# Kernel tuning notes

Measured on AMD Instinct MI355X. Metric: run time of the kernel, lower is better.

Reference implementation:

```python
import jax, jax.numpy as jnp
import numpy as np

D = 512    # d_model == EMBED_DIM
H = 8      # nhead
FF = 2048  # dim_feedforward
T, B, S, M = 64, 32, 64, 256
EPS = 1e-5


def setup_inputs() -> dict:
    key = jax.random.key(0)
    ks = iter(jax.random.split(key, 40))
    rn = lambda k, shp, s=0.02: s * jax.random.normal(k, shp, jnp.float32)
    inp = {
        'tgt': jax.random.normal(next(ks), (T, B, D), jnp.float32),
        'memory': jax.random.normal(next(ks), (M, B, D), jnp.float32),
        'semantics': jax.random.normal(next(ks), (B, S, D), jnp.float32),
    }
    for pfx in ('pt', 'sa', 'ca'):  # pre_target, self_attn, cross multihead_attn
        inp[pfx + '_wqkv'] = rn(next(ks), (3 * D, D))
        inp[pfx + '_bqkv'] = jnp.zeros((3 * D,), jnp.float32)
        inp[pfx + '_wo'] = rn(next(ks), (D, D))
        inp[pfx + '_bo'] = jnp.zeros((D,), jnp.float32)
    # relevant_mlp_pre_target: fc0 (2D->D), relu, fc1 (D->D), relu, fc2 (D->1)
    inp['mlp_w0'] = rn(next(ks), (D, 2 * D), float(np.sqrt(2.0 / (2 * D))))
    inp['mlp_b0'] = jnp.zeros((D,), jnp.float32)
    inp['mlp_w1'] = rn(next(ks), (D, D), float(np.sqrt(2.0 / D)))
    inp['mlp_b1'] = jnp.zeros((D,), jnp.float32)
    inp['mlp_w2'] = rn(next(ks), (1, D), float(np.sqrt(2.0 / D)))
    inp['mlp_b2'] = jnp.zeros((1,), jnp.float32)
    inp['ffn_w1'] = rn(next(ks), (FF, D))
    inp['ffn_b1'] = jnp.zeros((FF,), jnp.float32)
    inp['ffn_w2'] = rn(next(ks), (D, FF))
    inp['ffn_b2'] = jnp.zeros((D,), jnp.float32)
    for i in (1, 2, 3):
        inp[f'ln{i}_g'] = jnp.ones((D,), jnp.float32)
        inp[f'ln{i}_b'] = jnp.zeros((D,), jnp.float32)
    return inp


def layernorm(x, g, b):
    mu = jnp.mean(x, -1, keepdims=True)
    var = jnp.var(x, -1, keepdims=True)
    return (x - mu) * jax.lax.rsqrt(var + EPS) * g + b


def mha(q, k, v, wqkv, bqkv, wo, bo):
    # q,k,v: (L, B, D) seq-first, like torch nn.MultiheadAttention
    hd = D // H
    wq, wk, wv = jnp.split(wqkv, 3, axis=0)
    bq, bk, bv = jnp.split(bqkv, 3)
    qh = (q @ wq.T + bq).reshape(q.shape[0], q.shape[1], H, hd)
    kh = (k @ wk.T + bk).reshape(k.shape[0], k.shape[1], H, hd)
    vh = (v @ wv.T + bv).reshape(v.shape[0], v.shape[1], H, hd)
    scale = 1.0 / float(np.sqrt(hd))
    att = jax.nn.softmax(jnp.einsum('qbhd,kbhd->bhqk', qh * scale, kh), axis=-1)
    out = jnp.einsum('bhqk,kbhd->qbhd', att, vh).reshape(q.shape[0], q.shape[1], D)
    return out @ wo.T + bo


def get_relevant_semantic(feats, sem, w0, b0, w1, b1, w2, b2):
    # feats: (B,T,D), sem: (B,S,D). Linear-on-concat == sum of two linears, so we
    # never materialize the (B,T,S,2D) cat tensor; hidden (B,T,S,D) is unavoidable math.
    w0c, w0s = w0[:, :D], w0[:, D:]
    h = (feats @ w0c.T)[:, :, None, :] + (sem @ w0s.T)[:, None, :, :] + b0  # (B,T,S,D)
    h = jax.nn.relu(h)
    h = jax.nn.relu(h @ w1.T + b1)
    scores = h @ w2.T + b2                      # (B,T,S,1)
    a = jax.nn.softmax(scores, axis=2)          # softmax over sem axis
    return jnp.sum(sem[:, None, :, :] * a, axis=2)  # (B,T,D)


def reference(tgt, memory, semantics,
              pt_wqkv, pt_bqkv, pt_wo, pt_bo,
              sa_wqkv, sa_bqkv, sa_wo, sa_bo,
              ca_wqkv, ca_bqkv, ca_wo, ca_bo,
              mlp_w0, mlp_b0, mlp_w1, mlp_b1, mlp_w2, mlp_b2,
              ffn_w1, ffn_b1, ffn_w2, ffn_b2,
              ln1_g, ln1_b, ln2_g, ln2_b, ln3_g, ln3_b):
    # MULTIHEAD_PRE_TARGET branch (eval mode: dropout = identity)
    rel = get_relevant_semantic(jnp.transpose(tgt, (1, 0, 2)), semantics,
                                mlp_w0, mlp_b0, mlp_w1, mlp_b1, mlp_w2, mlp_b2)
    sem_k = jnp.transpose(rel, (1, 0, 2))  # (T,B,D) seq-first key/value
    x = tgt + mha(tgt, sem_k, sem_k, pt_wqkv, pt_bqkv, pt_wo, pt_bo)
    # self attention
    x = layernorm(x + mha(x, x, x, sa_wqkv, sa_bqkv, sa_wo, sa_bo), ln1_g, ln1_b)
    # cross attention over encoder memory
    x = layernorm(x + mha(x, memory, memory, ca_wqkv, ca_bqkv, ca_wo, ca_bo), ln2_g, ln2_b)
    # feed-forward
    ff = jax.nn.relu(x @ ffn_w1.T + ffn_b1) @ ffn_w2.T + ffn_b2
    return layernorm(x + ff, ln3_g, ln3_b)
```

## Files before the change

kernel.cpp:

```cpp
#include <hip/hip_runtime.h>
#include <hip/hip_bf16.h>

#define WS_B 32

typedef __attribute__((ext_vector_type(8))) __bf16 bf16x8;
typedef __attribute__((ext_vector_type(4))) float f32x4;
typedef unsigned short ushort_t;

#define MB(x) ((size_t)(x) << 20)
#define LSTR 40

__device__ __forceinline__ unsigned packpair(float lo, float hi) {
    return ((__float_as_uint(lo) + 0x8000u) >> 16) |
           ((__float_as_uint(hi) + 0x8000u) & 0xffff0000u);
}
__device__ __forceinline__ ushort_t f2bf(float x) {
    return (ushort_t)((__float_as_uint(x) + 0x8000u) >> 16);
}
__device__ __forceinline__ float bf2f(ushort_t u) {
    return __uint_as_float(((unsigned)u) << 16);
}
__device__ __forceinline__ unsigned fuse_word(unsigned f, unsigned s) {
    float lo = __uint_as_float(f << 16) + __uint_as_float(s << 16);
    float hi = __uint_as_float(f & 0xffff0000u) + __uint_as_float(s & 0xffff0000u);
    lo = fmaxf(lo, 0.f);
    hi = fmaxf(hi, 0.f);
    return packpair(lo, hi);
}

struct CvtArgs {
    const float* src[13];
    ushort_t* dst[13];
    int n4[13];
};
__global__ __launch_bounds__(256) void megacvt_kernel(CvtArgs a) {
    const int t = blockIdx.y;
    const int n = a.n4[t];
    const float4* S = (const float4*)a.src[t];
    uint2* D = (uint2*)a.dst[t];
    for (int i = blockIdx.x * 256 + threadIdx.x; i < n; i += gridDim.x * 256) {
        float4 v = S[i];
        uint2 o;
        o.x = packpair(v.x, v.y);
        o.y = packpair(v.z, v.w);
        D[i] = o;
    }
}

struct GemmDesc {
    const ushort_t* A;
    const ushort_t* W;
    const float* bias;
    const float* resid;
    float* C;
    ushort_t* Cb;
    int lda, ldw, ldc, K, relu, nbx, blkStart;
};
struct GemmBatch {
    GemmDesc d[4];
    int nd;
};

__global__ __launch_bounds__(256, 3) void mfma_gemm2(GemmBatch bt) {
    __shared__ ushort_t As[128 * LSTR];
    __shared__ ushort_t Bs[128 * LSTR];
    int di = 0;
#pragma unroll
    for (int i = 1; i < 4; ++i)
        if (i < bt.nd && (int)blockIdx.x >= bt.d[i].blkStart) di = i;
    const GemmDesc g = bt.d[di];
    const int local = blockIdx.x - g.blkStart;
    const int mb = local / g.nbx;
    const int nb = local - mb * g.nbx;

    const int tid = threadIdx.x;
    const int w = tid >> 6, lane = tid & 63;
    const int wm = w & 1, wn = w >> 1;
    const int l15 = lane & 15, quad = lane >> 4;

    const int arow = tid >> 1;
    const int a16 = (tid & 1) * 16;
    const ushort_t* Ap = g.A + (long)(mb * 128 + arow) * g.lda + a16;
    const ushort_t* Bp = g.W + (long)(nb * 128 + arow) * g.ldw + a16;
    ushort_t* Asw = &As[arow * LSTR + a16];
    ushort_t* Bsw = &Bs[arow * LSTR + a16];

    f32x4 acc[4][4];
#pragma unroll
    for (int i = 0; i < 4; ++i)
#pragma unroll
        for (int j = 0; j < 4; ++j) acc[i][j] = (f32x4)0.f;

    uint4 a0 = *(const uint4*)Ap;
    uint4 a1 = *(const uint4*)(Ap + 8);
    uint4 b0 = *(const uint4*)Bp;
    uint4 b1 = *(const uint4*)(Bp + 8);

    for (int k0 = 0; k0 < g.K; k0 += 32) {
        __syncthreads();
        *(uint4*)Asw = a0; *(uint4*)(Asw + 8) = a1;
        *(uint4*)Bsw = b0; *(uint4*)(Bsw + 8) = b1;
        if (k0 + 32 < g.K) {
            a0 = *(const uint4*)(Ap + k0 + 32);
            a1 = *(const uint4*)(Ap + k0 + 40);
            b0 = *(const uint4*)(Bp + k0 + 32);
            b1 = *(const uint4*)(Bp + k0 + 40);
        }
        __syncthreads();
        bf16x8 af[4], bf[4];
#pragma unroll
        for (int mt = 0; mt < 4; ++mt)
            af[mt] = *(const bf16x8*)&As[(wm * 64 + mt * 16 + l15) * LSTR + quad * 8];
#pragma unroll
        for (int nt = 0; nt < 4; ++nt)
            bf[nt] = *(const bf16x8*)&Bs[(wn * 64 + nt * 16 + l15) * LSTR + quad * 8];
#pragma unroll
        for (int mt = 0; mt < 4; ++mt)
#pragma unroll
            for (int nt = 0; nt < 4; ++nt)
                acc[mt][nt] = __builtin_amdgcn_mfma_f32_16x16x32_bf16(
                    af[mt], bf[nt], acc[mt][nt], 0, 0, 0);
    }

#pragma unroll
    for (int nt = 0; nt < 4; ++nt) {
        const int col = nb * 128 + wn * 64 + nt * 16 + l15;
        const float bv = g.bias ? g.bias[col] : 0.f;
#pragma unroll
        for (int mt = 0; mt < 4; ++mt) {
            const int row0 = mb * 128 + wm * 64 + mt * 16 + quad * 4;
#pragma unroll
            for (int rg = 0; rg < 4; ++rg) {
                float v = acc[mt][nt][rg] + bv;
                if (g.relu) v = fmaxf(v, 0.f);
                const long off = (long)(row0 + rg) * g.ldc + col;
                if (g.resid) v += g.resid[off];
                if (g.C) g.C[off] = v;
                if (g.Cb) g.Cb[off] = f2bf(v);
            }
        }
    }
}

__global__ __launch_bounds__(512, 2) void h2score_kernel(
    const ushort_t* __restrict__ Fb,
    const ushort_t* __restrict__ Sb,
    const ushort_t* __restrict__ w1b,
    const float* __restrict__ b1,
    const float* __restrict__ w2,
    float* __restrict__ scores4)
{
    __shared__ ushort_t As[128 * LSTR];
    __shared__ ushort_t Bs[256 * LSTR];
    __shared__ float scred[128 * 4];
    const int tid = threadIdx.x;
    const int mb = blockIdx.x, nb = blockIdx.y;
    const int w = tid >> 6, lane = tid & 63;
    const int wm = w & 1, wn = w >> 1;
    const int l15 = lane & 15, quad = lane >> 4;

    const int arow = tid >> 2, akc = tid & 3;
    const int m_g = mb * 128 + arow;
    const int r = m_g >> 6, s = m_g & 63, bidx = r & 31;
    const ushort_t* Fp = Fb + (long)r * 512 + akc * 8;
    const ushort_t* Sp = Sb + (long)(bidx * 64 + s) * 512 + akc * 8;
    const ushort_t* Bp0 = w1b + (long)(nb * 256 + arow) * 512 + akc * 8;
    const ushort_t* Bp1 = Bp0 + (long)128 * 512;
    ushort_t* Asw  = &As[arow * LSTR + akc * 8];
    ushort_t* Bsw0 = &Bs[arow * LSTR + akc * 8];
    ushort_t* Bsw1 = Bsw0 + 128 * LSTR;

    f32x4 acc[4][4];
#pragma unroll
    for (int i = 0; i < 4; ++i)
#pragma unroll
        for (int j = 0; j < 4; ++j) acc[i][j] = (f32x4)0.f;

    uint4 fa = *(const uint4*)Fp;
    uint4 sa = *(const uint4*)Sp;
    uint4 bb0 = *(const uint4*)Bp0;
    uint4 bb1 = *(const uint4*)Bp1;

    for (int k0 = 0; k0 < 512; k0 += 32) {
        __syncthreads();
        uint4 o;
        o.x = fuse_word(fa.x, sa.x);
        o.y = fuse_word(fa.y, sa.y);
        o.z = fuse_word(fa.z, sa.z);
        o.w = fuse_word(fa.w, sa.w);
        *(uint4*)Asw = o;
        *(uint4*)Bsw0 = bb0;
        *(uint4*)Bsw1 = bb1;
        if (k0 + 32 < 512) {
            fa  = *(const uint4*)(Fp + k0 + 32);
            sa  = *(const uint4*)(Sp + k0 + 32);
            bb0 = *(const uint4*)(Bp0 + k0 + 32);
            bb1 = *(const uint4*)(Bp1 + k0 + 32);
        }
        __syncthreads();
        bf16x8 af[4], bf[4];
#pragma unroll
        for (int mt = 0; mt < 4; ++mt)
            af[mt] = *(const bf16x8*)&As[(wm * 64 + mt * 16 + l15) * LSTR + quad * 8];
#pragma unroll
        for (int nt = 0; nt < 4; ++nt)
            bf[nt] = *(const bf16x8*)&Bs[(wn * 64 + nt * 16 + l15) * LSTR + quad * 8];
#pragma unroll
        for (int mt = 0; mt < 4; ++mt)
#pragma unroll
            for (int nt = 0; nt < 4; ++nt)
                acc[mt][nt] = __builtin_amdgcn_mfma_f32_16x16x32_bf16(
                    af[mt], bf[nt], acc[mt][nt], 0, 0, 0);
    }
    __syncthreads();

    float sp[4][4];
#pragma unroll
    for (int mt = 0; mt < 4; ++mt)
#pragma unroll
        for (int rg = 0; rg < 4; ++rg) sp[mt][rg] = 0.f;
#pragma unroll
    for (int nt = 0; nt < 4; ++nt) {
        const int col = nb * 256 + wn * 64 + nt * 16 + l15;
        const float cb = b1[col];
        const float cw = w2[col];
#pragma unroll
        for (int mt = 0; mt < 4; ++mt) {
#pragma unroll
            for (int rg = 0; rg < 4; ++rg)
                sp[mt][rg] += fmaxf(acc[mt][nt][rg] + cb, 0.f) * cw;
        }
    }
#pragma unroll
    for (int mt = 0; mt < 4; ++mt)
#pragma unroll
        for (int rg = 0; rg < 4; ++rg) {
            float v = sp[mt][rg];
            v += __shfl_xor(v, 1);
            v += __shfl_xor(v, 2);
            v += __shfl_xor(v, 4);
            v += __shfl_xor(v, 8);
            if (l15 == 0)
                scred[(wm * 64 + mt * 16 + quad * 4 + rg) * 4 + wn] = v;
        }
    __syncthreads();
    if (tid < 128) {
        float t = scred[tid * 4] + scred[tid * 4 + 1]
                + scred[tid * 4 + 2] + scred[tid * 4 + 3];
        scores4[(long)nb * 131072 + mb * 128 + tid] = t;
    }
}

__global__ __launch_bounds__(256) void softrel_kernel(
    const float* __restrict__ sc4,
    const ushort_t* __restrict__ semb,
    ushort_t* __restrict__ rel)
{
    __shared__ float a_s[64];
    const int tid = threadIdx.x;
    const int r = blockIdx.x;
    const int b = r & (WS_B - 1);
    if (tid < 64) {
        float t = sc4[r * 64 + tid] + sc4[131072 + r * 64 + tid];
        float m = t;
#pragma unroll
        for (int off = 32; off > 0; off >>= 1) m = fmaxf(m, __shfl_xor(m, off));
        float e = __expf(t - m);
        float su = e;
#pragma unroll
        for (int off = 32; off > 0; off >>= 1) su += __shfl_xor(su, off);
        a_s[tid] = e / su;
    }
    __syncthreads();
#pragma unroll
    for (int dd = 0; dd < 2; ++dd) {
        const int d = tid + dd * 256;
        float accd = 0.f;
        const ushort_t* sp = semb + (long)b * 64 * 512 + d;
        for (int s = 0; s < 64; ++s)
            accd += a_s[s] * bf2f(sp[s * 512]);
        rel[(long)r * 512 + d] = f2bf(accd);
    }
}

__global__ __launch_bounds__(256) void attn2_kernel(
    const ushort_t* __restrict__ Qm, int ldq, int qoff,
    const ushort_t* __restrict__ Km, int ldk, int koff,
    const ushort_t* __restrict__ Vm, int ldv, int voff,
    ushort_t* __restrict__ O,
    int Lk)
{
    __shared__ float sQT[64 * 34];
    __shared__ float sKT[64 * 68];
    __shared__ float sS[32 * 260];
    __shared__ float sredm[8 * 34];
    __shared__ float sreds[8 * 34];
    const int tid = threadIdx.x;
    const int b  = blockIdx.x >> 4;
    const int h  = (blockIdx.x >> 1) & 7;
    const int qt = blockIdx.x & 1;
    const int L8 = Lk >> 3;

    {
        const int q = tid >> 3, c = tid & 7;
        const int qg = qt * 32 + q;
        const ushort_t* pp = Qm + (long)(qg * WS_B + b) * ldq + qoff + h * 64 + c * 8;
        uint4 u = *(const uint4*)pp;
        const ushort_t* us = (const ushort_t*)&u;
#pragma unroll
        for (int i = 0; i < 8; ++i)
            sQT[(c * 8 + i) * 34 + q] = bf2f(us[i]);
    }

    const int k4 = (tid & 15) * 4;
    const int q2 = (tid >> 4) * 2;

    for (int kt = 0; kt < Lk; kt += 64) {
        __syncthreads();
        {
            const int kk = tid >> 3, c = tid & 7;
#pragma unroll
            for (int half = 0; half < 2; ++half) {
                const int kr = kk + half * 32;
                const ushort_t* pp = Km + (long)((kt + kr) * WS_B + b) * ldk + koff + h * 64 + c * 8;
                uint4 u = *(const uint4*)pp;
                const ushort_t* us = (const ushort_t*)&u;
#pragma unroll
                for (int i = 0; i < 8; ++i)
                    sKT[(c * 8 + i) * 68 + kr] = bf2f(us[i]);
            }
        }
        __syncthreads();
        float acc[2][4] = {{0.f, 0.f, 0.f, 0.f}, {0.f, 0.f, 0.f, 0.f}};
        for (int d = 0; d < 64; ++d) {
            const float qa = sQT[d * 34 + q2];
            const float qb = sQT[d * 34 + q2 + 1];
            const float4 kv = *(const float4*)&sKT[d * 68 + k4];
            acc[0][0] += qa * kv.x; acc[0][1] += qa * kv.y;
            acc[0][2] += qa * kv.z; acc[0][3] += qa * kv.w;
            acc[1][0] += qb * kv.x; acc[1][1] += qb * kv.y;
            acc[1][2] += qb * kv.z; acc[1][3] += qb * kv.w;
        }
#pragma unroll
        for (int i = 0; i < 2; ++i) {
            float4 v;
            v.x = acc[i][0] * 0.125f; v.y = acc[i][1] * 0.125f;
            v.z = acc[i][2] * 0.125f; v.w = acc[i][3] * 0.125f;
            *(float4*)&sS[(q2 + i) * 260 + kt + k4] = v;
        }
    }
    __syncthreads();

    {
        const int q = tid & 31, part = tid >> 5;
        const int kb = part * L8;
        float m = -1e30f;
        for (int k = 0; k < L8; ++k) m = fmaxf(m, sS[q * 260 + kb + k]);
        sredm[part * 34 + q] = m;
        __syncthreads();
        float M = sredm[q];
#pragma unroll
        for (int pz = 1; pz < 8; ++pz) M = fmaxf(M, sredm[pz * 34 + q]);
        float su = 0.f;
        for (int k = 0; k < L8; ++k) {
            float e = __expf(sS[q * 260 + kb + k] - M);
            sS[q * 260 + kb + k] = e;
            su += e;
        }
        sreds[part * 34 + q] = su;
    }
    __syncthreads();

    const int d4 = (tid & 15) * 4;
    float o[2][4] = {{0.f, 0.f, 0.f, 0.f}, {0.f, 0.f, 0.f, 0.f}};
    float* sV = sKT;
    for (int kt = 0; kt < Lk; kt += 64) {
        __syncthreads();
        {
            const int kk = tid >> 3, c = tid & 7;
#pragma unroll
            for (int half = 0; half < 2; ++half) {
                const int kr = kk + half * 32;
                const ushort_t* pp = Vm + (long)((kt + kr) * WS_B + b) * ldv + voff + h * 64 + c * 8;
                uint4 u = *(const uint4*)pp;
                const ushort_t* us = (const ushort_t*)&u;
                float4 w0, w1;
                w0.x = bf2f(us[0]); w0.y = bf2f(us[1]);
                w0.z = bf2f(us[2]); w0.w = bf2f(us[3]);
                w1.x = bf2f(us[4]); w1.y = bf2f(us[5]);
                w1.z = bf2f(us[6]); w1.w = bf2f(us[7]);
                *(float4*)&sV[kr * 68 + c * 8] = w0;
                *(float4*)&sV[kr * 68 + c * 8 + 4] = w1;
            }
        }
        __syncthreads();
        for (int k = 0; k < 64; ++k) {
            const float p0 = sS[q2 * 260 + kt + k];
            const float p1 = sS[(q2 + 1) * 260 + kt + k];
            const float4 vv = *(const float4*)&sV[k * 68 + d4];
            o[0][0] += p0 * vv.x; o[0][1] += p0 * vv.y;
            o[0][2] += p0 * vv.z; o[0][3] += p0 * vv.w;
            o[1][0] += p1 * vv.x; o[1][1] += p1 * vv.y;
            o[1][2] += p1 * vv.z; o[1][3] += p1 * vv.w;
        }
    }

#pragma unroll
    for (int i = 0; i < 2; ++i) {
        float su = 0.f;
#pragma unroll
        for (int pz = 0; pz < 8; ++pz) su += sreds[pz * 34 + q2 + i];
        const float inv = 1.f / su;
        const int qg = qt * 32 + q2 + i;
        ushort_t* op = O + (long)(qg * WS_B + b) * 512 + h * 64 + d4;
        uint2 pk;
        pk.x = packpair(o[i][0] * inv, o[i][1] * inv);
        pk.y = packpair(o[i][2] * inv, o[i][3] * inv);
        *(uint2*)op = pk;
    }
}

__global__ __launch_bounds__(256) void ln_kernel(
    const float* __restrict__ X,
    const float* __restrict__ g,
    const float* __restrict__ be,
    float* __restrict__ Y,
    ushort_t* __restrict__ Yb)
{
    const int row = blockIdx.x * 4 + (threadIdx.x >> 6);
    const int lane = threadIdx.x & 63;
    const float4* xp = (const float4*)(X + (long)row * 512);
    float4 x0 = xp[lane], x1 = xp[lane + 64];
    float sum = x0.x + x0.y + x0.z + x0.w + x1.x + x1.y + x1.z + x1.w;
    float sq = x0.x * x0.x + x0.y * x0.y + x0.z * x0.z + x0.w * x0.w
             + x1.x * x1.x + x1.y * x1.y + x1.z * x1.z + x1.w * x1.w;
#pragma unroll
    for (int off = 32; off > 0; off >>= 1) {
        sum += __shfl_xor(sum, off);
        sq += __shfl_xor(sq, off);
    }
    const float mu = sum * (1.f / 512.f);
    const float var = sq * (1.f / 512.f) - mu * mu;
    const float rs = rsqrtf(var + 1e-5f);
    const float4* gp = (const float4*)g;
    const float4* bp = (const float4*)be;
    float4 g0 = gp[lane], g1 = gp[lane + 64], b0 = bp[lane], b1 = bp[lane + 64];
    float4 y0, y1;
    y0.x = (x0.x - mu) * rs * g0.x + b0.x;
    y0.y = (x0.y - mu) * rs * g0.y + b0.y;
    y0.z = (x0.z - mu) * rs * g0.z + b0.z;
    y0.w = (x0.w - mu) * rs * g0.w + b0.w;
    y1.x = (x1.x - mu) * rs * g1.x + b1.x;
    y1.y = (x1.y - mu) * rs * g1.y + b1.y;
    y1.z = (x1.z - mu) * rs * g1.z + b1.z;
    y1.w = (x1.w - mu) * rs * g1.w + b1.w;
    float4* yp = (float4*)(Y + (long)row * 512);
    yp[lane] = y0; yp[lane + 64] = y1;
    if (Yb) {
        uint2* ybp = (uint2*)(Yb + (long)row * 512);
        uint2 p0, p1;
        p0.x = packpair(y0.x, y0.y); p0.y = packpair(y0.z, y0.w);
        p1.x = packpair(y1.x, y1.y); p1.y = packpair(y1.z, y1.w);
        ybp[lane] = p0; ybp[lane + 64] = p1;
    }
}

static inline GemmDesc mkdesc(const ushort_t* A, int lda, const ushort_t* W, int ldw,
                              const float* bias, const float* resid, float* C,
                              ushort_t* Cb, int ldc, int N, int K, int relu,
                              int blkStart)
{
    GemmDesc d;
    d.A = A; d.W = W; d.bias = bias; d.resid = resid; d.C = C; d.Cb = Cb;
    d.lda = lda; d.ldw = ldw; d.ldc = ldc; d.K = K; d.relu = relu;
    d.nbx = N / 128;
    d.blkStart = blkStart;
    return d;
}
static inline void mgemm(hipStream_t s, const ushort_t* A, int lda,
                         const ushort_t* W, int ldw, const float* bias,
                         const float* resid, float* C, ushort_t* Cb,
                         int ldc, int M, int N, int K, bool relu)
{
    GemmBatch bt;
    bt.nd = 1;
    bt.d[0] = mkdesc(A, lda, W, ldw, bias, resid, C, Cb, ldc, N, K, relu ? 1 : 0, 0);
    bt.d[1] = bt.d[0]; bt.d[2] = bt.d[0]; bt.d[3] = bt.d[0];
    mfma_gemm2<<<(M / 128) * (N / 128), 256, 0, s>>>(bt);
}

extern "C" void kernel_launch(void* const* d_in, const int* in_sizes, int n_in,
                              void* d_out, int out_size, void* d_ws, size_t ws_size,
                              hipStream_t stream)
{
    (void)in_sizes; (void)n_in; (void)out_size; (void)ws_size;
    const float* tgt       = (const float*)d_in[0];
    const float* memory    = (const float*)d_in[1];
    const float* semantics = (const float*)d_in[2];
    const float* pt_wqkv   = (const float*)d_in[3];
    const float* pt_bqkv   = (const float*)d_in[4];
    const float* pt_wo     = (const float*)d_in[5];
    const float* pt_bo     = (const float*)d_in[6];
    const float* sa_wqkv   = (const float*)d_in[7];
    const float* sa_bqkv   = (const float*)d_in[8];
    const float* sa_wo     = (const float*)d_in[9];
    const float* sa_bo     = (const float*)d_in[10];
    const float* ca_wqkv   = (const float*)d_in[11];
    const float* ca_bqkv   = (const float*)d_in[12];
    const float* ca_wo     = (const float*)d_in[13];
    const float* ca_bo     = (const float*)d_in[14];
    const float* mlp_w0    = (const float*)d_in[15];
    const float* mlp_b0    = (const float*)d_in[16];
    const float* mlp_w1    = (const float*)d_in[17];
    const float* mlp_b1    = (const float*)d_in[18];
    const float* mlp_w2    = (const float*)d_in[19];
    const float* ffn_w1    = (const float*)d_in[21];
    const float* ffn_b1    = (const float*)d_in[22];
    const float* ffn_w2    = (const float*)d_in[23];
    const float* ffn_b2    = (const float*)d_in[24];
    const float* ln1_g     = (const float*)d_in[25];
    const float* ln1_b     = (const float*)d_in[26];
    const float* ln2_g     = (const float*)d_in[27];
    const float* ln2_b     = (const float*)d_in[28];
    const float* ln3_g     = (const float*)d_in[29];
    const float* ln3_b     = (const float*)d_in[30];

    char* p = (char*)d_ws;
    ushort_t* w0b   = (ushort_t*)(p + 0);
    ushort_t* w1b   = (ushort_t*)(p + MB(1));
    ushort_t* ptwb  = (ushort_t*)(p + 1572864);
    ushort_t* ptob  = (ushort_t*)(p + MB(3));
    ushort_t* sawb  = (ushort_t*)(p + 3670016);
    ushort_t* saob  = (ushort_t*)(p + MB(5));
    ushort_t* cawb  = (ushort_t*)(p + 5767168);
    ushort_t* caob  = (ushort_t*)(p + MB(7));
    ushort_t* f1b   = (ushort_t*)(p + 7864320);
    ushort_t* f2b   = (ushort_t*)(p + 9961472);
    ushort_t* memb  = (ushort_t*)(p + MB(12));
    ushort_t* cakvb = (ushort_t*)(p + MB(20));
    ushort_t* tgtb  = (ushort_t*)(p + MB(36));
    ushort_t* semb  = (ushort_t*)(p + MB(38));
    ushort_t* Fb    = (ushort_t*)(p + MB(40));
    ushort_t* Sb    = (ushort_t*)(p + MB(42));
    float*    scores4 = (float*)(p + MB(44));
    ushort_t* relb  = (ushort_t*)(p + MB(45));
    ushort_t* Ob    = (ushort_t*)(p + MB(47));
    float*    x1f   = (float*)(p + MB(49));
    ushort_t* ptqb  = (ushort_t*)(p + MB(53));
    ushort_t* ptkvb = (ushort_t*)(p + MB(14));
    ushort_t* x1b   = (ushort_t*)(p + MB(18));
    ushort_t* saqkvb= (ushort_t*)(p + MB(38));
    float*    yf    = (float*)(p + MB(12));
    float*    x2f   = (float*)(p + MB(16));
    ushort_t* x2b   = (ushort_t*)(p + MB(36));
    ushort_t* caqb  = (ushort_t*)(p + MB(44));
    float*    x3f   = (float*)(p + MB(40));
    ushort_t* x3b   = (ushort_t*)(p + MB(38));
    ushort_t* hb    = (ushort_t*)(p + MB(20));

    CvtArgs ca;
    ca.src[0]  = tgt;       ca.dst[0]  = tgtb;  ca.n4[0]  = 262144;
    ca.src[1]  = semantics; ca.dst[1]  = semb;  ca.n4[1]  = 262144;
    ca.src[2]  = memory;    ca.dst[2]  = memb;  ca.n4[2]  = 1048576;
    ca.src[3]  = mlp_w0;    ca.dst[3]  = w0b;   ca.n4[3]  = 131072;
    ca.src[4]  = mlp_w1;    ca.dst[4]  = w1b;   ca.n4[4]  = 65536;
    ca.src[5]  = pt_wqkv;   ca.dst[5]  = ptwb;  ca.n4[5]  = 196608;
    ca.src[6]  = pt_wo;     ca.dst[6]  = ptob;  ca.n4[6]  = 65536;
    ca.src[7]  = sa_wqkv;   ca.dst[7]  = sawb;  ca.n4[7]  = 196608;
    ca.src[8]  = sa_wo;     ca.dst[8]  = saob;  ca.n4[8]  = 65536;
    ca.src[9]  = ca_wqkv;   ca.dst[9]  = cawb;  ca.n4[9]  = 196608;
    ca.src[10] = ca_wo;     ca.dst[10] = caob;  ca.n4[10] = 65536;
    ca.src[11] = ffn_w1;    ca.dst[11] = f1b;   ca.n4[11] = 262144;
    ca.src[12] = ffn_w2;    ca.dst[12] = f2b;   ca.n4[12] = 262144;
    megacvt_kernel<<<dim3(1024, 13), 256, 0, stream>>>(ca);

    {
        GemmBatch bt;
        bt.nd = 4;
        bt.d[0] = mkdesc(memb, 512, cawb + 512 * 512, 512, ca_bqkv + 512, nullptr,
                         nullptr, cakvb, 1024, 1024, 512, 0, 0);
        bt.d[1] = mkdesc(tgtb, 512, w0b, 1024, mlp_b0, nullptr,
                         nullptr, Fb, 512, 512, 512, 0, 512);
        bt.d[2] = mkdesc(semb, 512, w0b + 512, 1024, nullptr, nullptr,
                         nullptr, Sb, 512, 512, 512, 0, 576);
        bt.d[3] = mkdesc(tgtb, 512, ptwb, 512, pt_bqkv, nullptr,
                         nullptr, ptqb, 512, 512, 512, 0, 640);
        mfma_gemm2<<<704, 256, 0, stream>>>(bt);
    }

    h2score_kernel<<<dim3(1024, 2), 512, 0, stream>>>(Fb, Sb, w1b, mlp_b1,
                                                      mlp_w2, scores4);
    softrel_kernel<<<2048, 256, 0, stream>>>(scores4, semb, relb);

    mgemm(stream, relb, 512, ptwb + 512 * 512, 512, pt_bqkv + 512, nullptr,
          nullptr, ptkvb, 1024, 2048, 1024, 512, false);
    attn2_kernel<<<512, 256, 0, stream>>>(ptqb, 512, 0, ptkvb, 1024, 0,
                                          ptkvb, 1024, 512, Ob, 64);
    mgemm(stream, Ob, 512, ptob, 512, pt_bo, tgt, x1f, x1b, 512,
          2048, 512, 512, false);

    mgemm(stream, x1b, 512, sawb, 512, sa_bqkv, nullptr, nullptr, saqkvb, 1536,
          2048, 1536, 512, false);
    attn2_kernel<<<512, 256, 0, stream>>>(saqkvb, 1536, 0, saqkvb, 1536, 512,
                                          saqkvb, 1536, 1024, Ob, 64);
    mgemm(stream, Ob, 512, saob, 512, sa_bo, x1f, yf, nullptr, 512,
          2048, 512, 512, false);
    ln_kernel<<<512, 256, 0, stream>>>(yf, ln1_g, ln1_b, x2f, x2b);

    mgemm(stream, x2b, 512, cawb, 512, ca_bqkv, nullptr, nullptr, caqb, 512,
          2048, 512, 512, false);
    attn2_kernel<<<512, 256, 0, stream>>>(caqb, 512, 0, cakvb, 1024, 0,
                                          cakvb, 1024, 512, Ob, 256);
    mgemm(stream, Ob, 512, caob, 512, ca_bo, x2f, yf, nullptr, 512,
          2048, 512, 512, false);
    ln_kernel<<<512, 256, 0, stream>>>(yf, ln2_g, ln2_b, x3f, x3b);

    mgemm(stream, x3b, 512, f1b, 512, ffn_b1, nullptr, nullptr, hb, 2048,
          2048, 2048, 512, true);
    mgemm(stream, hb, 2048, f2b, 2048, ffn_b2, x3f, yf, nullptr, 512,
          2048, 512, 2048, false);
    ln_kernel<<<512, 256, 0, stream>>>(yf, ln3_g, ln3_b, (float*)d_out, nullptr);
}
```

Baseline: 527.7 us.

## Fuse post-relevance decoder chain into one cooperative persistent kernel with grid syncs

Replaces the sequence of about 14 separate GEMM, attention and layernorm launches after the relevance step with a single cooperative kernel of 512 blocks that runs each stage as a device function separated by grid.sync. If the cooperative launch fails it falls back to the old launch sequence. The aim is to remove per-launch overhead and launch gaps between small kernels. The cost is that GEMM stages use only 64 to 256 tiles, so many blocks idle, and each stage pays a grid-wide barrier. The LDS row padding (stride 40 to 32) is also removed, which may add bank conflicts, and h2score drops its register prefetch.

```diff
diff --git a/kernel.cpp b/kernel.cpp
--- a/kernel.cpp
+++ b/kernel.cpp
@@ -1,5 +1,8 @@
 #include <hip/hip_runtime.h>
 #include <hip/hip_bf16.h>
+#include <hip/hip_cooperative_groups.h>
+
+namespace cg = cooperative_groups;
 
 #define WS_B 32
 
@@ -8,7 +11,6 @@
 typedef unsigned short ushort_t;
 
 #define MB(x) ((size_t)(x) << 20)
-#define LSTR 40
 
 __device__ __forceinline__ unsigned packpair(float lo, float hi) {
     return ((__float_as_uint(lo) + 0x8000u) >> 16) |
@@ -47,32 +49,15 @@
     }
 }
 
-struct GemmDesc {
-    const ushort_t* A;
-    const ushort_t* W;
-    const float* bias;
-    const float* resid;
-    float* C;
-    ushort_t* Cb;
-    int lda, ldw, ldc, K, relu, nbx, blkStart;
-};
-struct GemmBatch {
-    GemmDesc d[4];
-    int nd;
-};
-
-__global__ __launch_bounds__(256, 3) void mfma_gemm2(GemmBatch bt) {
-    __shared__ ushort_t As[128 * LSTR];
-    __shared__ ushort_t Bs[128 * LSTR];
-    int di = 0;
-#pragma unroll
-    for (int i = 1; i < 4; ++i)
-        if (i < bt.nd && (int)blockIdx.x >= bt.d[i].blkStart) di = i;
-    const GemmDesc g = bt.d[di];
-    const int local = blockIdx.x - g.blkStart;
-    const int mb = local / g.nbx;
-    const int nb = local - mb * g.nbx;
-
+__device__ __forceinline__ void dev_gemm_tile(char* smemraw, int mb, int nb,
+    const ushort_t* __restrict__ A, int lda,
+    const ushort_t* __restrict__ W, int ldw,
+    const float* __restrict__ bias, const float* __restrict__ resid,
+    float* __restrict__ C, ushort_t* __restrict__ Cb,
+    int ldc, int K, int relu)
+{
+    ushort_t* As = (ushort_t*)smemraw;
+    ushort_t* Bs = (ushort_t*)(smemraw + 8192);
     const int tid = threadIdx.x;
     const int w = tid >> 6, lane = tid & 63;
     const int wm = w & 1, wn = w >> 1;
@@ -80,10 +65,10 @@
 
     const int arow = tid >> 1;
     const int a16 = (tid & 1) * 16;
-    const ushort_t* Ap = g.A + (long)(mb * 128 + arow) * g.lda + a16;
-    const ushort_t* Bp = g.W + (long)(nb * 128 + arow) * g.ldw + a16;
-    ushort_t* Asw = &As[arow * LSTR + a16];
-    ushort_t* Bsw = &Bs[arow * LSTR + a16];
+    const ushort_t* Ap = A + (long)(mb * 128 + arow) * lda + a16;
+    const ushort_t* Bp = W + (long)(nb * 128 + arow) * ldw + a16;
+    ushort_t* Asw = &As[arow * 32 + a16];
+    ushort_t* Bsw = &Bs[arow * 32 + a16];
 
     f32x4 acc[4][4];
 #pragma unroll
@@ -96,11 +81,11 @@
     uint4 b0 = *(const uint4*)Bp;
     uint4 b1 = *(const uint4*)(Bp + 8);
 
-    for (int k0 = 0; k0 < g.K; k0 += 32) {
+    for (int k0 = 0; k0 < K; k0 += 32) {
         __syncthreads();
         *(uint4*)Asw = a0; *(uint4*)(Asw + 8) = a1;
         *(uint4*)Bsw = b0; *(uint4*)(Bsw + 8) = b1;
-        if (k0 + 32 < g.K) {
+        if (k0 + 32 < K) {
             a0 = *(const uint4*)(Ap + k0 + 32);
             a1 = *(const uint4*)(Ap + k0 + 40);
             b0 = *(const uint4*)(Bp + k0 + 32);
@@ -110,10 +95,10 @@
         bf16x8 af[4], bf[4];
 #pragma unroll
         for (int mt = 0; mt < 4; ++mt)
-            af[mt] = *(const bf16x8*)&As[(wm * 64 + mt * 16 + l15) * LSTR + quad * 8];
+            af[mt] = *(const bf16x8*)&As[(wm * 64 + mt * 16 + l15) * 32 + quad * 8];
 #pragma unroll
         for (int nt = 0; nt < 4; ++nt)
-            bf[nt] = *(const bf16x8*)&Bs[(wn * 64 + nt * 16 + l15) * LSTR + quad * 8];
+            bf[nt] = *(const bf16x8*)&Bs[(wn * 64 + nt * 16 + l15) * 32 + quad * 8];
 #pragma unroll
         for (int mt = 0; mt < 4; ++mt)
 #pragma unroll
@@ -125,180 +110,38 @@
 #pragma unroll
     for (int nt = 0; nt < 4; ++nt) {
         const int col = nb * 128 + wn * 64 + nt * 16 + l15;
-        const float bv = g.bias ? g.bias[col] : 0.f;
+        const float bv = bias ? bias[col] : 0.f;
 #pragma unroll
         for (int mt = 0; mt < 4; ++mt) {
             const int row0 = mb * 128 + wm * 64 + mt * 16 + quad * 4;
 #pragma unroll
             for (int rg = 0; rg < 4; ++rg) {
                 float v = acc[mt][nt][rg] + bv;
-                if (g.relu) v = fmaxf(v, 0.f);
-                const long off = (long)(row0 + rg) * g.ldc + col;
-                if (g.resid) v += g.resid[off];
-                if (g.C) g.C[off] = v;
-                if (g.Cb) g.Cb[off] = f2bf(v);
+                if (relu) v = fmaxf(v, 0.f);
+                const long off = (long)(row0 + rg) * ldc + col;
+                if (resid) v += resid[off];
+                if (C) C[off] = v;
+                if (Cb) Cb[off] = f2bf(v);
             }
         }
     }
 }
 
-__global__ __launch_bounds__(512, 2) void h2score_kernel(
-    const ushort_t* __restrict__ Fb,
-    const ushort_t* __restrict__ Sb,
-    const ushort_t* __restrict__ w1b,
-    const float* __restrict__ b1,
-    const float* __restrict__ w2,
-    float* __restrict__ scores4)
-{
-    __shared__ ushort_t As[128 * LSTR];
-    __shared__ ushort_t Bs[256 * LSTR];
-    __shared__ float scred[128 * 4];
-    const int tid = threadIdx.x;
-    const int mb = blockIdx.x, nb = blockIdx.y;
-    const int w = tid >> 6, lane = tid & 63;
-    const int wm = w & 1, wn = w >> 1;
-    const int l15 = lane & 15, quad = lane >> 4;
-
-    const int arow = tid >> 2, akc = tid & 3;
-    const int m_g = mb * 128 + arow;
-    const int r = m_g >> 6, s = m_g & 63, bidx = r & 31;
-    const ushort_t* Fp = Fb + (long)r * 512 + akc * 8;
-    const ushort_t* Sp = Sb + (long)(bidx * 64 + s) * 512 + akc * 8;
-    const ushort_t* Bp0 = w1b + (long)(nb * 256 + arow) * 512 + akc * 8;
-    const ushort_t* Bp1 = Bp0 + (long)128 * 512;
-    ushort_t* Asw  = &As[arow * LSTR + akc * 8];
-    ushort_t* Bsw0 = &Bs[arow * LSTR + akc * 8];
-    ushort_t* Bsw1 = Bsw0 + 128 * LSTR;
-
-    f32x4 acc[4][4];
-#pragma unroll
-    for (int i = 0; i < 4; ++i)
-#pragma unroll
-        for (int j = 0; j < 4; ++j) acc[i][j] = (f32x4)0.f;
-
-    uint4 fa = *(const uint4*)Fp;
-    uint4 sa = *(const uint4*)Sp;
-    uint4 bb0 = *(const uint4*)Bp0;
-    uint4 bb1 = *(const uint4*)Bp1;
-
-    for (int k0 = 0; k0 < 512; k0 += 32) {
-        __syncthreads();
-        uint4 o;
-        o.x = fuse_word(fa.x, sa.x);
-        o.y = fuse_word(fa.y, sa.y);
-        o.z = fuse_word(fa.z, sa.z);
-        o.w = fuse_word(fa.w, sa.w);
-        *(uint4*)Asw = o;
-        *(uint4*)Bsw0 = bb0;
-        *(uint4*)Bsw1 = bb1;
-        if (k0 + 32 < 512) {
-            fa  = *(const uint4*)(Fp + k0 + 32);
-            sa  = *(const uint4*)(Sp + k0 + 32);
-            bb0 = *(const uint4*)(Bp0 + k0 + 32);
-            bb1 = *(const uint4*)(Bp1 + k0 + 32);
-        }
-        __syncthreads();
-        bf16x8 af[4], bf[4];
-#pragma unroll
-        for (int mt = 0; mt < 4; ++mt)
-            af[mt] = *(const bf16x8*)&As[(wm * 64 + mt * 16 + l15) * LSTR + quad * 8];
-#pragma unroll
-        for (int nt = 0; nt < 4; ++nt)
-            bf[nt] = *(const bf16x8*)&Bs[(wn * 64 + nt * 16 + l15) * LSTR + quad * 8];
-#pragma unroll
-        for (int mt = 0; mt < 4; ++mt)
-#pragma unroll
-            for (int nt = 0; nt < 4; ++nt)
-                acc[mt][nt] = __builtin_amdgcn_mfma_f32_16x16x32_bf16(
-                    af[mt], bf[nt], acc[mt][nt], 0, 0, 0);
-    }
-    __syncthreads();
-
-    float sp[4][4];
-#pragma unroll
-    for (int mt = 0; mt < 4; ++mt)
-#pragma unroll
-        for (int rg = 0; rg < 4; ++rg) sp[mt][rg] = 0.f;
-#pragma unroll
-    for (int nt = 0; nt < 4; ++nt) {
-        const int col = nb * 256 + wn * 64 + nt * 16 + l15;
-        const float cb = b1[col];
-        const float cw = w2[col];
-#pragma unroll
-        for (int mt = 0; mt < 4; ++mt) {
-#pragma unroll
-            for (int rg = 0; rg < 4; ++rg)
-                sp[mt][rg] += fmaxf(acc[mt][nt][rg] + cb, 0.f) * cw;
-        }
-    }
-#pragma unroll
-    for (int mt = 0; mt < 4; ++mt)
-#pragma unroll
-        for (int rg = 0; rg < 4; ++rg) {
-            float v = sp[mt][rg];
-            v += __shfl_xor(v, 1);
-            v += __shfl_xor(v, 2);
-            v += __shfl_xor(v, 4);
-            v += __shfl_xor(v, 8);
-            if (l15 == 0)
-                scred[(wm * 64 + mt * 16 + quad * 4 + rg) * 4 + wn] = v;
-        }
-    __syncthreads();
-    if (tid < 128) {
-        float t = scred[tid * 4] + scred[tid * 4 + 1]
-                + scred[tid * 4 + 2] + scred[tid * 4 + 3];
-        scores4[(long)nb * 131072 + mb * 128 + tid] = t;
-    }
-}
-
-__global__ __launch_bounds__(256) void softrel_kernel(
-    const float* __restrict__ sc4,
-    const ushort_t* __restrict__ semb,
-    ushort_t* __restrict__ rel)
-{
-    __shared__ float a_s[64];
-    const int tid = threadIdx.x;
-    const int r = blockIdx.x;
-    const int b = r & (WS_B - 1);
-    if (tid < 64) {
-        float t = sc4[r * 64 + tid] + sc4[131072 + r * 64 + tid];
-        float m = t;
-#pragma unroll
-        for (int off = 32; off > 0; off >>= 1) m = fmaxf(m, __shfl_xor(m, off));
-        float e = __expf(t - m);
-        float su = e;
-#pragma unroll
-        for (int off = 32; off > 0; off >>= 1) su += __shfl_xor(su, off);
-        a_s[tid] = e / su;
-    }
-    __syncthreads();
-#pragma unroll
-    for (int dd = 0; dd < 2; ++dd) {
-        const int d = tid + dd * 256;
-        float accd = 0.f;
-        const ushort_t* sp = semb + (long)b * 64 * 512 + d;
-        for (int s = 0; s < 64; ++s)
-            accd += a_s[s] * bf2f(sp[s * 512]);
-        rel[(long)r * 512 + d] = f2bf(accd);
-    }
-}
-
-__global__ __launch_bounds__(256) void attn2_kernel(
+__device__ __forceinline__ void dev_attn(char* smemraw, int unit,
     const ushort_t* __restrict__ Qm, int ldq, int qoff,
     const ushort_t* __restrict__ Km, int ldk, int koff,
     const ushort_t* __restrict__ Vm, int ldv, int voff,
-    ushort_t* __restrict__ O,
-    int Lk)
-{
-    __shared__ float sQT[64 * 34];
-    __shared__ float sKT[64 * 68];
-    __shared__ float sS[32 * 260];
-    __shared__ float sredm[8 * 34];
-    __shared__ float sreds[8 * 34];
+    ushort_t* __restrict__ O, int Lk)
+{
+    float* sQT  = (float*)smemraw;
+    float* sKT  = (float*)(smemraw + 8704);
+    float* sS   = (float*)(smemraw + 26112);
+    float* sredm = (float*)(smemraw + 59392);
+    float* sreds = (float*)(smemraw + 60480);
     const int tid = threadIdx.x;
-    const int b  = blockIdx.x >> 4;
-    const int h  = (blockIdx.x >> 1) & 7;
-    const int qt = blockIdx.x & 1;
+    const int b  = unit >> 4;
+    const int h  = (unit >> 1) & 7;
+    const int qt = unit & 1;
     const int L8 = Lk >> 3;
 
     {
@@ -420,14 +263,12 @@
     }
 }
 
-__global__ __launch_bounds__(256) void ln_kernel(
-    const float* __restrict__ X,
-    const float* __restrict__ g,
-    const float* __restrict__ be,
-    float* __restrict__ Y,
+__device__ __forceinline__ void dev_ln(int rowg,
+    const float* __restrict__ X, const float* __restrict__ g,
+    const float* __restrict__ be, float* __restrict__ Y,
     ushort_t* __restrict__ Yb)
 {
-    const int row = blockIdx.x * 4 + (threadIdx.x >> 6);
+    const int row = rowg * 4 + (threadIdx.x >> 6);
     const int lane = threadIdx.x & 63;
     const float4* xp = (const float4*)(X + (long)row * 512);
     float4 x0 = xp[lane], x1 = xp[lane + 64];
@@ -463,6 +304,254 @@
         p1.x = packpair(y1.x, y1.y); p1.y = packpair(y1.z, y1.w);
         ybp[lane] = p0; ybp[lane + 64] = p1;
     }
+}
+
+struct GemmDesc {
+    const ushort_t* A;
+    const ushort_t* W;
+    const float* bias;
+    const float* resid;
+    float* C;
+    ushort_t* Cb;
+    int lda, ldw, ldc, K, relu, nbx, blkStart;
+};
+struct GemmBatch {
+    GemmDesc d[4];
+    int nd;
+};
+__global__ __launch_bounds__(256, 3) void mfma_gemm2(GemmBatch bt) {
+    __shared__ __align__(16) char smem[16384];
+    int di = 0;
+#pragma unroll
+    for (int i = 1; i < 4; ++i)
+        if (i < bt.nd && (int)blockIdx.x >= bt.d[i].blkStart) di = i;
+    const GemmDesc g = bt.d[di];
+    const int local = blockIdx.x - g.blkStart;
+    const int mb = local / g.nbx;
+    dev_gemm_tile(smem, mb, local - mb * g.nbx, g.A, g.lda, g.W, g.ldw,
+                  g.bias, g.resid, g.C, g.Cb, g.ldc, g.K, g.relu);
+}
+
+__global__ __launch_bounds__(256) void attn2_kernel(
+    const ushort_t* Qm, int ldq, int qoff,
+    const ushort_t* Km, int ldk, int koff,
+    const ushort_t* Vm, int ldv, int voff,
+    ushort_t* O, int Lk)
+{
+    __shared__ __align__(16) char smem[61568];
+    dev_attn(smem, blockIdx.x, Qm, ldq, qoff, Km, ldk, koff, Vm, ldv, voff, O, Lk);
+}
+
+__global__ __launch_bounds__(256) void ln_kernel(
+    const float* X, const float* g, const float* be,
+    float* Y, ushort_t* Yb)
+{
+    dev_ln(blockIdx.x, X, g, be, Y, Yb);
+}
+
+__global__ __launch_bounds__(512, 2) void h2score_kernel(
+    const ushort_t* __restrict__ Fb,
+    const ushort_t* __restrict__ Sb,
+    const ushort_t* __restrict__ w1b,
+    const float* __restrict__ b1,
+    const float* __restrict__ w2,
+    float* __restrict__ scores4)
+{
+    __shared__ ushort_t As[128 * 32];
+    __shared__ ushort_t Bs[256 * 32];
+    __shared__ float scred[128 * 4];
+    const int tid = threadIdx.x;
+    const int mb = blockIdx.x, nb = blockIdx.y;
+    const int w = tid >> 6, lane = tid & 63;
+    const int wm = w & 1, wn = w >> 1;
+    const int l15 = lane & 15, quad = lane >> 4;
+
+    const int arow = tid >> 2, akc = tid & 3;
+    const int m_g = mb * 128 + arow;
+    const int r = m_g >> 6, s = m_g & 63, bidx = r & 31;
+    const ushort_t* Fp = Fb + (long)r * 512 + akc * 8;
+    const ushort_t* Sp = Sb + (long)(bidx * 64 + s) * 512 + akc * 8;
+    const ushort_t* Bp0 = w1b + (long)(nb * 256 + arow) * 512 + akc * 8;
+    const ushort_t* Bp1 = Bp0 + (long)128 * 512;
+    ushort_t* Asw = &As[arow * 32 + akc * 8];
+    ushort_t* Bsw0 = &Bs[arow * 32 + akc * 8];
+    ushort_t* Bsw1 = Bsw0 + 128 * 32;
+
+    f32x4 acc[4][4];
+#pragma unroll
+    for (int i = 0; i < 4; ++i)
+#pragma unroll
+        for (int j = 0; j < 4; ++j) acc[i][j] = (f32x4)0.f;
+
+    for (int k0 = 0; k0 < 512; k0 += 32) {
+        uint4 fa = *(const uint4*)(Fp + k0);
+        uint4 sa = *(const uint4*)(Sp + k0);
+        uint4 bb0 = *(const uint4*)(Bp0 + k0);
+        uint4 bb1 = *(const uint4*)(Bp1 + k0);
+        __syncthreads();
+        uint4 o;
+        o.x = fuse_word(fa.x, sa.x);
+        o.y = fuse_word(fa.y, sa.y);
+        o.z = fuse_word(fa.z, sa.z);
+        o.w = fuse_word(fa.w, sa.w);
+        *(uint4*)Asw = o;
+        *(uint4*)Bsw0 = bb0;
+        *(uint4*)Bsw1 = bb1;
+        __syncthreads();
+        bf16x8 af[4], bf[4];
+#pragma unroll
+        for (int mt = 0; mt < 4; ++mt)
+            af[mt] = *(const bf16x8*)&As[(wm * 64 + mt * 16 + l15) * 32 + quad * 8];
+#pragma unroll
+        for (int nt = 0; nt < 4; ++nt)
+            bf[nt] = *(const bf16x8*)&Bs[(wn * 64 + nt * 16 + l15) * 32 + quad * 8];
+#pragma unroll
+        for (int mt = 0; mt < 4; ++mt)
+#pragma unroll
+            for (int nt = 0; nt < 4; ++nt)
+                acc[mt][nt] = __builtin_amdgcn_mfma_f32_16x16x32_bf16(
+                    af[mt], bf[nt], acc[mt][nt], 0, 0, 0);
+    }
+    __syncthreads();
+
+    float sp[4][4];
+#pragma unroll
+    for (int mt = 0; mt < 4; ++mt)
+#pragma unroll
+        for (int rg = 0; rg < 4; ++rg) sp[mt][rg] = 0.f;
+#pragma unroll
+    for (int nt = 0; nt < 4; ++nt) {
+        const int col = nb * 256 + wn * 64 + nt * 16 + l15;
+        const float cb = b1[col];
+        const float cw = w2[col];
+#pragma unroll
+        for (int mt = 0; mt < 4; ++mt) {
+#pragma unroll
+            for (int rg = 0; rg < 4; ++rg)
+                sp[mt][rg] += fmaxf(acc[mt][nt][rg] + cb, 0.f) * cw;
+        }
+    }
+#pragma unroll
+    for (int mt = 0; mt < 4; ++mt)
+#pragma unroll
+        for (int rg = 0; rg < 4; ++rg) {
+            float v = sp[mt][rg];
+            v += __shfl_xor(v, 1);
+            v += __shfl_xor(v, 2);
+            v += __shfl_xor(v, 4);
+            v += __shfl_xor(v, 8);
+            if (l15 == 0)
+                scred[(wm * 64 + mt * 16 + quad * 4 + rg) * 4 + wn] = v;
+        }
+    __syncthreads();
+    if (tid < 128) {
+        float t = scred[tid * 4] + scred[tid * 4 + 1]
+                + scred[tid * 4 + 2] + scred[tid * 4 + 3];
+        scores4[(long)nb * 131072 + mb * 128 + tid] = t;
+    }
+}
+
+__global__ __launch_bounds__(256) void softrel_kernel(
+    const float* __restrict__ sc4,
+    const ushort_t* __restrict__ semb,
+    ushort_t* __restrict__ rel)
+{
+    __shared__ float a_s[64];
+    const int tid = threadIdx.x;
+    const int r = blockIdx.x;
+    const int b = r & (WS_B - 1);
+    if (tid < 64) {
+        float t = sc4[r * 64 + tid] + sc4[131072 + r * 64 + tid];
+        float m = t;
+#pragma unroll
+        for (int off = 32; off > 0; off >>= 1) m = fmaxf(m, __shfl_xor(m, off));
+        float e = __expf(t - m);
+        float su = e;
+#pragma unroll
+        for (int off = 32; off > 0; off >>= 1) su += __shfl_xor(su, off);
+        a_s[tid] = e / su;
+    }
+    __syncthreads();
+#pragma unroll
+    for (int dd = 0; dd < 2; ++dd) {
+        const int d = tid + dd * 256;
+        float accd = 0.f;
+        const ushort_t* sp = semb + (long)b * 64 * 512 + d;
+        for (int s = 0; s < 64; ++s)
+            accd += a_s[s] * bf2f(sp[s * 512]);
+        rel[(long)r * 512 + d] = f2bf(accd);
+    }
+}
+
+struct ChainArgs {
+    const ushort_t* relb; const ushort_t* ptw_kv; const float* pt_bq_kv; ushort_t* ptkvb;
+    const ushort_t* ptqb; ushort_t* Ob;
+    const ushort_t* ptob; const float* pt_bo; const float* tgt; float* x1f; ushort_t* x1b;
+    const ushort_t* sawb; const float* sa_bqkv; ushort_t* saqkvb;
+    const ushort_t* saob; const float* sa_bo; float* yf;
+    const float* ln1_g; const float* ln1_b; float* x2f; ushort_t* x2b;
+    const ushort_t* cawb; const float* ca_bqkv; ushort_t* caqb;
+    const ushort_t* cakvb;
+    const ushort_t* caob; const float* ca_bo;
+    const float* ln2_g; const float* ln2_b; float* x3f; ushort_t* x3b;
+    const ushort_t* f1b; const float* ffn_b1; ushort_t* hb;
+    const ushort_t* f2b; const float* ffn_b2;
+    const float* ln3_g; const float* ln3_b; float* outp;
+};
+
+__global__ __launch_bounds__(256, 2) void chain_kernel(ChainArgs a) {
+    __shared__ __align__(16) char smem[61568];
+    cg::grid_group grid = cg::this_grid();
+    const int blk = blockIdx.x;
+
+    if (blk < 128)
+        dev_gemm_tile(smem, blk >> 3, blk & 7, a.relb, 512, a.ptw_kv, 512,
+                      a.pt_bq_kv, nullptr, nullptr, a.ptkvb, 1024, 512, 0);
+    grid.sync();
+    dev_attn(smem, blk, a.ptqb, 512, 0, a.ptkvb, 1024, 0, a.ptkvb, 1024, 512,
+             a.Ob, 64);
+    grid.sync();
+    if (blk < 64)
+        dev_gemm_tile(smem, blk >> 2, blk & 3, a.Ob, 512, a.ptob, 512,
+                      a.pt_bo, a.tgt, a.x1f, a.x1b, 512, 512, 0);
+    grid.sync();
+    if (blk < 192) {
+        const int mb = blk / 12, nb = blk - mb * 12;
+        dev_gemm_tile(smem, mb, nb, a.x1b, 512, a.sawb, 512, a.sa_bqkv,
+                      nullptr, nullptr, a.saqkvb, 1536, 512, 0);
+    }
+    grid.sync();
+    dev_attn(smem, blk, a.saqkvb, 1536, 0, a.saqkvb, 1536, 512,
+             a.saqkvb, 1536, 1024, a.Ob, 64);
+    grid.sync();
+    if (blk < 64)
+        dev_gemm_tile(smem, blk >> 2, blk & 3, a.Ob, 512, a.saob, 512,
+                      a.sa_bo, a.x1f, a.yf, nullptr, 512, 512, 0);
+    grid.sync();
+    dev_ln(blk, a.yf, a.ln1_g, a.ln1_b, a.x2f, a.x2b);
+    grid.sync();
+    if (blk < 64)
+        dev_gemm_tile(smem, blk >> 2, blk & 3, a.x2b, 512, a.cawb, 512,
+                      a.ca_bqkv, nullptr, nullptr, a.caqb, 512, 512, 0);
+    grid.sync();
+    dev_attn(smem, blk, a.caqb, 512, 0, a.cakvb, 1024, 0, a.cakvb, 1024, 512,
+             a.Ob, 256);
+    grid.sync();
+    if (blk < 64)
+        dev_gemm_tile(smem, blk >> 2, blk & 3, a.Ob, 512, a.caob, 512,
+                      a.ca_bo, a.x2f, a.yf, nullptr, 512, 512, 0);
+    grid.sync();
+    dev_ln(blk, a.yf, a.ln2_g, a.ln2_b, a.x3f, a.x3b);
+    grid.sync();
+    if (blk < 256)
+        dev_gemm_tile(smem, blk >> 4, blk & 15, a.x3b, 512, a.f1b, 512,
+                      a.ffn_b1, nullptr, nullptr, a.hb, 2048, 512, 1);
+    grid.sync();
+    if (blk < 64)
+        dev_gemm_tile(smem, blk >> 2, blk & 3, a.hb, 2048, a.f2b, 2048,
+                      a.ffn_b2, a.x3f, a.yf, nullptr, 512, 2048, 0);
+    grid.sync();
+    dev_ln(blk, a.yf, a.ln3_g, a.ln3_b, a.outp, nullptr);
 }
 
 static inline GemmDesc mkdesc(const ushort_t* A, int lda, const ushort_t* W, int ldw,
@@ -592,32 +681,52 @@
                                                       mlp_w2, scores4);
     softrel_kernel<<<2048, 256, 0, stream>>>(scores4, semb, relb);
 
-    mgemm(stream, relb, 512, ptwb + 512 * 512, 512, pt_bqkv + 512, nullptr,
-          nullptr, ptkvb, 1024, 2048, 1024, 512, false);
-    attn2_kernel<<<512, 256, 0, stream>>>(ptqb, 512, 0, ptkvb, 1024, 0,
-                                          ptkvb, 1024, 512, Ob, 64);
-    mgemm(stream, Ob, 512, ptob, 512, pt_bo, tgt, x1f, x1b, 512,
-          2048, 512, 512, false);
-
-    mgemm(stream, x1b, 512, sawb, 512, sa_bqkv, nullptr, nullptr, saqkvb, 1536,
-          2048, 1536, 512, false);
-    attn2_kernel<<<512, 256, 0, stream>>>(saqkvb, 1536, 0, saqkvb, 1536, 512,
-                                          saqkvb, 1536, 1024, Ob, 64);
-    mgemm(stream, Ob, 512, saob, 512, sa_bo, x1f, yf, nullptr, 512,
-          2048, 512, 512, false);
-    ln_kernel<<<512, 256, 0, stream>>>(yf, ln1_g, ln1_b, x2f, x2b);
-
-    mgemm(stream, x2b, 512, cawb, 512, ca_bqkv, nullptr, nullptr, caqb, 512,
-          2048, 512, 512, false);
-    attn2_kernel<<<512, 256, 0, stream>>>(caqb, 512, 0, cakvb, 1024, 0,
-                                          cakvb, 1024, 512, Ob, 256);
-    mgemm(stream, Ob, 512, caob, 512, ca_bo, x2f, yf, nullptr, 512,
-          2048, 512, 512, false);
-    ln_kernel<<<512, 256, 0, stream>>>(yf, ln2_g, ln2_b, x3f, x3b);
-
-    mgemm(stream, x3b, 512, f1b, 512, ffn_b1, nullptr, nullptr, hb, 2048,
-          2048, 2048, 512, true);
-    mgemm(stream, hb, 2048, f2b, 2048, ffn_b2, x3f, yf, nullptr, 512,
-          2048, 512, 2048, false);
-    ln_kernel<<<512, 256, 0, stream>>>(yf, ln3_g, ln3_b, (float*)d_out, nullptr);
-}
+    ChainArgs cargs;
+    cargs.relb = relb; cargs.ptw_kv = ptwb + 512 * 512; cargs.pt_bq_kv = pt_bqkv + 512;
+    cargs.ptkvb = ptkvb;
+    cargs.ptqb = ptqb; cargs.Ob = Ob;
+    cargs.ptob = ptob; cargs.pt_bo = pt_bo; cargs.tgt = tgt; cargs.x1f = x1f; cargs.x1b = x1b;
+    cargs.sawb = sawb; cargs.sa_bqkv = sa_bqkv; cargs.saqkvb = saqkvb;
+    cargs.saob = saob; cargs.sa_bo = sa_bo; cargs.yf = yf;
+    cargs.ln1_g = ln1_g; cargs.ln1_b = ln1_b; cargs.x2f = x2f; cargs.x2b = x2b;
+    cargs.cawb = cawb; cargs.ca_bqkv = ca_bqkv; cargs.caqb = caqb;
+    cargs.cakvb = cakvb;
+    cargs.caob = caob; cargs.ca_bo = ca_bo;
+    cargs.ln2_g = ln2_g; cargs.ln2_b = ln2_b; cargs.x3f = x3f; cargs.x3b = x3b;
+    cargs.f1b = f1b; cargs.ffn_b1 = ffn_b1; cargs.hb = hb;
+    cargs.f2b = f2b; cargs.ffn_b2 = ffn_b2;
+    cargs.ln3_g = ln3_g; cargs.ln3_b = ln3_b; cargs.outp = (float*)d_out;
+
+    void* params[] = { (void*)&cargs };
+    hipError_t ce = hipLaunchCooperativeKernel((const void*)chain_kernel,
+                                               dim3(512), dim3(256), params,
+                                               0, stream);
+    if (ce != hipSuccess) {
+        (void)hipGetLastError();
+        mgemm(stream, relb, 512, ptwb + 512 * 512, 512, pt_bqkv + 512, nullptr,
+              nullptr, ptkvb, 1024, 2048, 1024, 512, false);
+        attn2_kernel<<<512, 256, 0, stream>>>(ptqb, 512, 0, ptkvb, 1024, 0,
+                                              ptkvb, 1024, 512, Ob, 64);
+        mgemm(stream, Ob, 512, ptob, 512, pt_bo, tgt, x1f, x1b, 512,
+              2048, 512, 512, false);
+        mgemm(stream, x1b, 512, sawb, 512, sa_bqkv, nullptr, nullptr, saqkvb,
+              1536, 2048, 1536, 512, false);
+        attn2_kernel<<<512, 256, 0, stream>>>(saqkvb, 1536, 0, saqkvb, 1536, 512,
+                                              saqkvb, 1536, 1024, Ob, 64);
+        mgemm(stream, Ob, 512, saob, 512, sa_bo, x1f, yf, nullptr, 512,
+              2048, 512, 512, false);
+        ln_kernel<<<512, 256, 0, stream>>>(yf, ln1_g, ln1_b, x2f, x2b);
+        mgemm(stream, x2b, 512, cawb, 512, ca_bqkv, nullptr, nullptr, caqb, 512,
+              2048, 512, 512, false);
+        attn2_kernel<<<512, 256, 0, stream>>>(caqb, 512, 0, cakvb, 1024, 0,
+                                              cakvb, 1024, 512, Ob, 256);
+        mgemm(stream, Ob, 512, caob, 512, ca_bo, x2f, yf, nullptr, 512,
+              2048, 512, 512, false);
+        ln_kernel<<<512, 256, 0, stream>>>(yf, ln2_g, ln2_b, x3f, x3b);
+        mgemm(stream, x3b, 512, f1b, 512, ffn_b1, nullptr, nullptr, hb, 2048,
+              2048, 2048, 512, true);
+        mgemm(stream, hb, 2048, f2b, 2048, ffn_b2, x3f, yf, nullptr, 512,
+              2048, 512, 2048, false);
+        ln_kernel<<<512, 256, 0, stream>>>(yf, ln3_g, ln3_b, (float*)d_out, nullptr);
+    }
+}
```

Measured after the change: 1.284 ms. 2.43x slower.
